# Kernel optimization log

Measured on AMD Instinct MI355X. Metric: run time of the kernel, lower is better.

Reference implementation:

```python
import jax, jax.numpy as jnp
import numpy as np

TEMPERATURE = 0.02
B, T, D = 32, 256, 128


def _l2norm(x):
    return x / jnp.linalg.norm(x, axis=-1, keepdims=True)


def setup_inputs() -> dict:
    key = jax.random.key(0)
    k1, k2, k3, k4, k5, k6 = jax.random.split(key, 6)
    query_single = _l2norm(jax.random.normal(k1, (B, D), dtype=jnp.float32))
    pos_single = _l2norm(jax.random.normal(k2, (B, D), dtype=jnp.float32))
    query_multi = _l2norm(jax.random.normal(k3, (B, T, D), dtype=jnp.float32))
    pos_multi = _l2norm(jax.random.normal(k4, (B, T, D), dtype=jnp.float32))
    # variable-length masks (at least 1 valid token each, like real tokenized batches)
    q_len = jax.random.randint(k5, (B,), T // 4, T + 1)
    p_len = jax.random.randint(k6, (B,), T // 4, T + 1)
    pos = jnp.arange(T)[None, :]
    q_mask = pos < q_len[:, None]
    p_mask = pos < p_len[:, None]
    return {
        "query_single": query_single,
        "pos_single": pos_single,
        "query_multi": query_multi,
        "pos_multi": pos_multi,
        "q_mask": q_mask,
        "p_mask": p_mask,
    }


def _late_interaction_similarity(q_tokens, q_mask, p_tokens, p_mask):
    # All-pairs token similarity: [Bq, Bp, Tq, Tp]
    sim = jnp.einsum("bqd,cpd->bcqp", q_tokens, p_tokens)
    neg = jnp.finfo(sim.dtype).min
    sim = jnp.where(p_mask[None, :, None, :], sim, neg)
    mx = jnp.max(sim, axis=-1)                       # [Bq, Bp, Tq]
    mx = jnp.where(q_mask[:, None, :], mx, 0.0)      # drop invalid query tokens
    s = jnp.sum(mx, axis=-1)                         # [Bq, Bp]
    t_i = jnp.maximum(jnp.sum(q_mask, axis=-1), 1).astype(sim.dtype)  # [Bq]
    return s / t_i[:, None]


def _diag_cross_entropy(logits):
    # labels = arange(B): standard in-batch InfoNCE
    logp = jax.nn.log_softmax(logits, axis=-1)
    return -jnp.mean(jnp.diagonal(logp))


def reference(query_single, pos_single, query_multi, pos_multi, q_mask, p_mask):
    tau = TEMPERATURE
    dense_sim = query_single @ pos_single.T                       # [B, B]
    single_loss = _diag_cross_entropy(dense_sim / tau)

    S_late = _late_interaction_similarity(query_multi, q_mask, pos_multi, p_mask)
    multi_loss = _diag_cross_entropy(S_late / tau)

    dense_probs = jax.nn.softmax(dense_sim / tau, axis=1)
    late_probs = jax.nn.softmax(S_late / tau, axis=1)
    eps = 1e-8
    kl = jnp.mean(jnp.sum(dense_probs * jnp.log((dense_probs + eps) / (late_probs + eps)), axis=1))

    total_loss = single_loss + multi_loss + kl
    return (total_loss, single_loss, multi_loss, kl)
```

## Files before the change

### kernel.cpp

```cpp
#include <hip/hip_runtime.h>
#include <hip/hip_bf16.h>

#define B_SZ 32
#define T_SZ 256
#define D_SZ 128
#define TAU_INV 50.0f

typedef __bf16 bf16x8 __attribute__((ext_vector_type(8)));
typedef float f32x4 __attribute__((ext_vector_type(4)));

__device__ __forceinline__ unsigned short f2bf(float f) {
    union { float f; unsigned int u; } v; v.f = f;
    unsigned int r = v.u + 0x7fffu + ((v.u >> 16) & 1u);
    return (unsigned short)(r >> 16);
}

__device__ __forceinline__ bool mask_is_byte(const void* m) {
    return ((const int*)m)[0] != 1;
}
__device__ __forceinline__ int mget(const void* m, int idx, bool isb) {
    return isb ? (((const unsigned char*)m)[idx] != 0) : (((const int*)m)[idx] != 0);
}

__global__ __launch_bounds__(256) void cvt_prep(
    const float* __restrict__ qsrc, const float* __restrict__ psrc,
    const void* __restrict__ qmask, const void* __restrict__ pmask,
    unsigned short* __restrict__ Qb, unsigned short* __restrict__ Pb,
    float* __restrict__ maddF, float* __restrict__ qmulF,
    int* __restrict__ p_hiA, float* __restrict__ tcntA) {
    const int tid = threadIdx.x;
    const int half = blockIdx.x >> 10;
    if (half < 2) {
        const float* s = half ? psrc : qsrc;
        unsigned short* d = half ? Pb : Qb;
        int i = ((blockIdx.x & 1023) * 256 + tid) * 4;
        float4 v = *(const float4*)(s + i);
        ushort4 o;
        o.x = f2bf(v.x); o.y = f2bf(v.y); o.z = f2bf(v.z); o.w = f2bf(v.w);
        *(ushort4*)(d + i) = o;
        return;
    }
    __shared__ int sl[4], sc[4];
    const bool isb = mask_is_byte(qmask);
    const int r = blockIdx.x - 2048;
    const int t = tid;
    const int pm = mget(pmask, r * T_SZ + t, isb);
    const int qm = mget(qmask, r * T_SZ + t, isb);
    maddF[r * T_SZ + t] = pm ? 0.0f : -1e30f;
    qmulF[r * T_SZ + t] = qm ? 1.0f : 0.0f;
    int lp = pm ? t + 1 : 0, cq = qm;
    #pragma unroll
    for (int off = 1; off < 64; off <<= 1) {
        int o = __shfl_xor(lp, off);
        lp = o > lp ? o : lp;
        cq += __shfl_xor(cq, off);
    }
    if ((tid & 63) == 0) { sl[tid >> 6] = lp; sc[tid >> 6] = cq; }
    __syncthreads();
    if (tid == 0) {
        int LP = sl[0], CQ = sc[0];
        #pragma unroll
        for (int i = 1; i < 4; ++i) { LP = sl[i] > LP ? sl[i] : LP; CQ += sc[i]; }
        p_hiA[r] = LP > 1 ? LP : 1;
        tcntA[r] = (float)(CQ > 1 ? CQ : 1);
    }
}

__global__ __launch_bounds__(512, 4) void late_sim(
    const unsigned short* __restrict__ Qbf, const unsigned short* __restrict__ Pbf,
    const float* __restrict__ maddF, const float* __restrict__ qmulF,
    const int* __restrict__ p_hiA, float* __restrict__ sraw)
{
    __shared__ __align__(16) unsigned char Plds[T_SZ * D_SZ * 2];
    __shared__ float madd[T_SZ];
    __shared__ float qmul[2][T_SZ];
    __shared__ float wsum[2][8];

    const int tid = threadIdx.x;
    const int l   = tid & 63;
    const int w   = tid >> 6;
    const int bid = blockIdx.x;
    const int xcd = bid & 7;
    const int idx = bid >> 3;
    const int bg  = xcd * 2 + (idx >> 5);
    const int c   = idx & 31;
    const int b0  = bg, b1 = bg + 16;
    const int lr  = l & 15;
    const int lg  = l >> 4;

    const int p_hi    = p_hiA[c];
    const int ptmax   = (p_hi + 15) >> 4;
    const int stiters = (p_hi + 31) >> 5;

    const int qrow = w * 32 + (l & 31);
    const bool do0 = __any(qmulF[b0 * T_SZ + qrow] > 0.0f);
    const bool do1 = __any(qmulF[b1 * T_SZ + qrow] > 0.0f);

    bf16x8 qf0[2][4] = {}, qf1[2][4] = {};
    if (do0)
        #pragma unroll
        for (int qt = 0; qt < 2; ++qt)
            #pragma unroll
            for (int k = 0; k < 4; ++k)
                qf0[qt][k] = *(const bf16x8*)(Qbf + b0 * (T_SZ * D_SZ)
                              + (w * 32 + qt * 16 + lr) * D_SZ + k * 32 + lg * 8);
    if (do1)
        #pragma unroll
        for (int qt = 0; qt < 2; ++qt)
            #pragma unroll
            for (int k = 0; k < 4; ++k)
                qf1[qt][k] = *(const bf16x8*)(Qbf + b1 * (T_SZ * D_SZ)
                              + (w * 32 + qt * 16 + lr) * D_SZ + k * 32 + lg * 8);

    {
        const unsigned short* Pc = Pbf + c * (T_SZ * D_SZ);
        for (int it = 0; it < stiters; ++it) {
            int j   = it * 512 + w * 64 + l;
            int row = j >> 4;
            int cj  = j & 15;
            const unsigned short* src = Pc + row * D_SZ + ((cj ^ (row & 7)) << 3);
            __builtin_amdgcn_global_load_lds(
                (const __attribute__((address_space(1))) unsigned int*)src,
                (__attribute__((address_space(3))) unsigned int*)(Plds + (it * 512 + w * 64) * 16),
                16, 0, 0);
        }
    }
    if (tid < 64) {
        *(float4*)(madd + tid * 4) = *(const float4*)(maddF + c * T_SZ + tid * 4);
    } else if (tid < 128) {
        int t = tid - 64;
        *(float4*)(qmul[0] + t * 4) = *(const float4*)(qmulF + b0 * T_SZ + t * 4);
    } else if (tid < 192) {
        int t = tid - 128;
        *(float4*)(qmul[1] + t * 4) = *(const float4*)(qmulF + b1 * T_SZ + t * 4);
    }
    __syncthreads();

    float r00 = -3e38f, r01 = -3e38f, r10 = -3e38f, r11 = -3e38f;

    for (int pt = 0; pt < ptmax; ++pt) {
        f32x4 a00 = {0,0,0,0}, a01 = {0,0,0,0}, a10 = {0,0,0,0}, a11 = {0,0,0,0};
        #pragma unroll
        for (int k = 0; k < 4; ++k) {
            int row = pt * 16 + lr;
            bf16x8 af = *(const bf16x8*)(Plds + row * 256 + (((k * 4 + lg) ^ (row & 7)) << 4));
            if (do0) {
                a00 = __builtin_amdgcn_mfma_f32_16x16x32_bf16(af, qf0[0][k], a00, 0, 0, 0);
                a01 = __builtin_amdgcn_mfma_f32_16x16x32_bf16(af, qf0[1][k], a01, 0, 0, 0);
            }
            if (do1) {
                a10 = __builtin_amdgcn_mfma_f32_16x16x32_bf16(af, qf1[0][k], a10, 0, 0, 0);
                a11 = __builtin_amdgcn_mfma_f32_16x16x32_bf16(af, qf1[1][k], a11, 0, 0, 0);
            }
        }
        float pm0 = madd[pt * 16 + lg * 4 + 0];
        float pm1 = madd[pt * 16 + lg * 4 + 1];
        float pm2 = madd[pt * 16 + lg * 4 + 2];
        float pm3v = madd[pt * 16 + lg * 4 + 3];
        if (do0) {
            r00 = fmaxf(r00, fmaxf(fmaxf(a00[0]+pm0, a00[1]+pm1), fmaxf(a00[2]+pm2, a00[3]+pm3v)));
            r01 = fmaxf(r01, fmaxf(fmaxf(a01[0]+pm0, a01[1]+pm1), fmaxf(a01[2]+pm2, a01[3]+pm3v)));
        }
        if (do1) {
            r10 = fmaxf(r10, fmaxf(fmaxf(a10[0]+pm0, a10[1]+pm1), fmaxf(a10[2]+pm2, a10[3]+pm3v)));
            r11 = fmaxf(r11, fmaxf(fmaxf(a11[0]+pm0, a11[1]+pm1), fmaxf(a11[2]+pm2, a11[3]+pm3v)));
        }
    }

    r00 = fmaxf(r00, __shfl_xor(r00, 16)); r00 = fmaxf(r00, __shfl_xor(r00, 32));
    r01 = fmaxf(r01, __shfl_xor(r01, 16)); r01 = fmaxf(r01, __shfl_xor(r01, 32));
    r10 = fmaxf(r10, __shfl_xor(r10, 16)); r10 = fmaxf(r10, __shfl_xor(r10, 32));
    r11 = fmaxf(r11, __shfl_xor(r11, 16)); r11 = fmaxf(r11, __shfl_xor(r11, 32));

    float t0 = r00 * qmul[0][w * 32 + lr] + r01 * qmul[0][w * 32 + 16 + lr];
    float t1 = r10 * qmul[1][w * 32 + lr] + r11 * qmul[1][w * 32 + 16 + lr];
    #pragma unroll
    for (int off = 32; off > 0; off >>= 1) {
        t0 += __shfl_down(t0, off);
        t1 += __shfl_down(t1, off);
    }
    if (l == 0) { wsum[0][w] = t0 * 0.25f; wsum[1][w] = t1 * 0.25f; }
    __syncthreads();

    if (tid == 0) {
        float s0 = 0.f, s1 = 0.f;
        #pragma unroll
        for (int ww = 0; ww < 8; ++ww) { s0 += wsum[0][ww]; s1 += wsum[1][ww]; }
        sraw[b0 * 32 + c] = s0;
        sraw[b1 * 32 + c] = s1;
    }
}

__global__ __launch_bounds__(256) void loss_row(
    const float* __restrict__ qs, const float* __restrict__ ps,
    const float* __restrict__ sraw, const float* __restrict__ tcntA,
    float* __restrict__ out)
{
    __shared__ float denseL[B_SZ], lateL[B_SZ];
    const int r   = blockIdx.x;
    const int tid = threadIdx.x;
    const int cc  = tid >> 3;
    const int j   = tid & 7;

    {
        const float4* qa = (const float4*)(qs + r  * D_SZ + j * 16);
        const float4* pb = (const float4*)(ps + cc * D_SZ + j * 16);
        float s = 0.f;
        #pragma unroll
        for (int v = 0; v < 4; ++v) {
            float4 q = qa[v], p = pb[v];
            s += q.x * p.x + q.y * p.y + q.z * p.z + q.w * p.w;
        }
        s += __shfl_xor(s, 1);
        s += __shfl_xor(s, 2);
        s += __shfl_xor(s, 4);
        if (j == 0) denseL[cc] = s;
    }
    if (tid < B_SZ) lateL[tid] = sraw[r * 32 + tid] / tcntA[r];
    __syncthreads();

    if (tid >= 32) return;
    const int lane = tid;
    float xd = denseL[lane] * TAU_INV;
    float xl = lateL[lane]  * TAU_INV;
    float md = xd, ml = xl;
    #pragma unroll
    for (int off = 16; off > 0; off >>= 1) {
        md = fmaxf(md, __shfl_xor(md, off));
        ml = fmaxf(ml, __shfl_xor(ml, off));
    }
    float sd = expf(xd - md), sl = expf(xl - ml);
    #pragma unroll
    for (int off = 16; off > 0; off >>= 1) {
        sd += __shfl_xor(sd, off);
        sl += __shfl_xor(sl, off);
    }
    float lsd = md + logf(sd);
    float lsl = ml + logf(sl);
    float pd = expf(xd - lsd);
    float pl = expf(xl - lsl);
    float klt = pd * logf((pd + 1e-8f) / (pl + 1e-8f));
    #pragma unroll
    for (int off = 16; off > 0; off >>= 1) klt += __shfl_xor(klt, off);

    float logpd = xd - lsd;
    float logpl = xl - lsl;
    float dlogd = __shfl(logpd, r);
    float dlogl = __shfl(logpl, r);

    if (lane == 0) {
        const float inv = 1.0f / (float)B_SZ;
        float a = -dlogd * inv;
        float b = -dlogl * inv;
        float k = klt * inv;
        atomicAdd(out + 1, a);
        atomicAdd(out + 2, b);
        atomicAdd(out + 3, k);
        atomicAdd(out + 0, a + b + k);
    }
}

extern "C" void kernel_launch(void* const* d_in, const int* in_sizes, int n_in,
                              void* d_out, int out_size, void* d_ws, size_t ws_size,
                              hipStream_t stream) {
    const float* qs    = (const float*)d_in[0];
    const float* ps    = (const float*)d_in[1];
    const float* qm3   = (const float*)d_in[2];
    const float* pm3   = (const float*)d_in[3];
    const void*  qmask = d_in[4];
    const void*  pmask = d_in[5];
    float* out = (float*)d_out;

    const int NTOK = B_SZ * T_SZ * D_SZ;
    unsigned short* Qbf = (unsigned short*)d_ws;
    unsigned short* Pbf = Qbf + NTOK;
    float* sraw  = (float*)(Pbf + NTOK);
    float* maddF = sraw + 1024;
    float* qmulF = maddF + B_SZ * T_SZ;
    int*   p_hiA = (int*)(qmulF + B_SZ * T_SZ);
    float* tcntA = (float*)(p_hiA + 32);

    hipMemsetAsync(out, 0, 4 * sizeof(float), stream);
    cvt_prep<<<2080, 256, 0, stream>>>(qm3, pm3, qmask, pmask, Qbf, Pbf,
                                       maddF, qmulF, p_hiA, tcntA);
    late_sim<<<512, 512, 0, stream>>>(Qbf, Pbf, maddF, qmulF, p_hiA, sraw);
    loss_row<<<B_SZ, 256, 0, stream>>>(qs, ps, sraw, tcntA, out);
}
```

Measured before the change: 35.73 us.

## Double-buffer two passage blocks per workgroup and coarsen bf16 conversion

The late-interaction kernel now uses 1024-thread workgroups that handle two passage batches each. Each wave covers one query batch, and the second passage tile is loaded into a separate LDS buffer while the first is being computed. The conversion kernel handles eight elements of both Q and P per thread, which cuts the block count. Two 64KB LDS buffers limit occupancy to one block per CU, and the grid shrinks to 256 blocks, which may reduce latency hiding.

Result: faster. 34.28 us, median of 2 (-4.1%).

```diff
diff --git a/kernel.cpp b/kernel.cpp
--- a/kernel.cpp
+++ b/kernel.cpp
@@ -22,27 +22,31 @@
     return isb ? (((const unsigned char*)m)[idx] != 0) : (((const int*)m)[idx] != 0);
 }
 
-__global__ __launch_bounds__(256) void cvt_prep(
+__global__ __launch_bounds__(256) void cvt_prep2(
     const float* __restrict__ qsrc, const float* __restrict__ psrc,
     const void* __restrict__ qmask, const void* __restrict__ pmask,
     unsigned short* __restrict__ Qb, unsigned short* __restrict__ Pb,
     float* __restrict__ maddF, float* __restrict__ qmulF,
     int* __restrict__ p_hiA, float* __restrict__ tcntA) {
     const int tid = threadIdx.x;
-    const int half = blockIdx.x >> 10;
-    if (half < 2) {
-        const float* s = half ? psrc : qsrc;
-        unsigned short* d = half ? Pb : Qb;
-        int i = ((blockIdx.x & 1023) * 256 + tid) * 4;
-        float4 v = *(const float4*)(s + i);
-        ushort4 o;
-        o.x = f2bf(v.x); o.y = f2bf(v.y); o.z = f2bf(v.z); o.w = f2bf(v.w);
-        *(ushort4*)(d + i) = o;
+    if (blockIdx.x < 512) {
+        int i = (blockIdx.x * 256 + tid) * 8;
+        const float4* q4 = (const float4*)(qsrc + i);
+        const float4* p4 = (const float4*)(psrc + i);
+        float4 a0 = q4[0], a1 = q4[1], b0 = p4[0], b1 = p4[1];
+        ushort4 oq0 = { f2bf(a0.x), f2bf(a0.y), f2bf(a0.z), f2bf(a0.w) };
+        ushort4 oq1 = { f2bf(a1.x), f2bf(a1.y), f2bf(a1.z), f2bf(a1.w) };
+        ushort4 op0 = { f2bf(b0.x), f2bf(b0.y), f2bf(b0.z), f2bf(b0.w) };
+        ushort4 op1 = { f2bf(b1.x), f2bf(b1.y), f2bf(b1.z), f2bf(b1.w) };
+        *(ushort4*)(Qb + i)     = oq0;
+        *(ushort4*)(Qb + i + 4) = oq1;
+        *(ushort4*)(Pb + i)     = op0;
+        *(ushort4*)(Pb + i + 4) = op1;
         return;
     }
     __shared__ int sl[4], sc[4];
     const bool isb = mask_is_byte(qmask);
-    const int r = blockIdx.x - 2048;
+    const int r = blockIdx.x - 512;
     const int t = tid;
     const int pm = mget(pmask, r * T_SZ + t, isb);
     const int qm = mget(qmask, r * T_SZ + t, isb);
@@ -66,104 +70,131 @@
     }
 }
 
-__global__ __launch_bounds__(512, 4) void late_sim(
+__global__ __launch_bounds__(1024, 4) void late_sim2(
     const unsigned short* __restrict__ Qbf, const unsigned short* __restrict__ Pbf,
     const float* __restrict__ maddF, const float* __restrict__ qmulF,
     const int* __restrict__ p_hiA, float* __restrict__ sraw)
 {
-    __shared__ __align__(16) unsigned char Plds[T_SZ * D_SZ * 2];
-    __shared__ float madd[T_SZ];
-    __shared__ float qmul[2][T_SZ];
-    __shared__ float wsum[2][8];
+    __shared__ __align__(16) unsigned char Pl[2][T_SZ * D_SZ * 2];
+    __shared__ float maddL[2][T_SZ];
+    __shared__ float qmulL[2][T_SZ];
+    __shared__ float wsum[16][2];
 
     const int tid = threadIdx.x;
     const int l   = tid & 63;
     const int w   = tid >> 6;
     const int bid = blockIdx.x;
     const int xcd = bid & 7;
-    const int idx = bid >> 3;
-    const int bg  = xcd * 2 + (idx >> 5);
-    const int c   = idx & 31;
+    const int j   = bid >> 3;
+    const int bg  = xcd * 2 + (j >> 4);
+    const int cp  = j & 15;
+    const int c0  = cp * 2, c1 = cp * 2 + 1;
     const int b0  = bg, b1 = bg + 16;
     const int lr  = l & 15;
     const int lg  = l >> 4;
-
-    const int p_hi    = p_hiA[c];
-    const int ptmax   = (p_hi + 15) >> 4;
-    const int stiters = (p_hi + 31) >> 5;
-
-    const int qrow = w * 32 + (l & 31);
-    const bool do0 = __any(qmulF[b0 * T_SZ + qrow] > 0.0f);
-    const bool do1 = __any(qmulF[b1 * T_SZ + qrow] > 0.0f);
-
-    bf16x8 qf0[2][4] = {}, qf1[2][4] = {};
-    if (do0)
+    const int wb  = w >> 3;
+    const int myb = wb ? b1 : b0;
+    const int s   = (w & 7) * 32;
+
+    const int p_hi0 = p_hiA[c0], p_hi1 = p_hiA[c1];
+    const int pt0 = (p_hi0 + 15) >> 4, st0 = (p_hi0 + 63) >> 6;
+    const int pt1 = (p_hi1 + 15) >> 4, st1 = (p_hi1 + 63) >> 6;
+
+    const bool dob = __any(qmulF[myb * T_SZ + s + (l & 31)] > 0.0f);
+
+    bf16x8 qf[2][4] = {};
+    if (dob)
         #pragma unroll
         for (int qt = 0; qt < 2; ++qt)
             #pragma unroll
             for (int k = 0; k < 4; ++k)
-                qf0[qt][k] = *(const bf16x8*)(Qbf + b0 * (T_SZ * D_SZ)
-                              + (w * 32 + qt * 16 + lr) * D_SZ + k * 32 + lg * 8);
-    if (do1)
-        #pragma unroll
-        for (int qt = 0; qt < 2; ++qt)
-            #pragma unroll
-            for (int k = 0; k < 4; ++k)
-                qf1[qt][k] = *(const bf16x8*)(Qbf + b1 * (T_SZ * D_SZ)
-                              + (w * 32 + qt * 16 + lr) * D_SZ + k * 32 + lg * 8);
+                qf[qt][k] = *(const bf16x8*)(Qbf + myb * (T_SZ * D_SZ)
+                              + (s + qt * 16 + lr) * D_SZ + k * 32 + lg * 8);
 
     {
-        const unsigned short* Pc = Pbf + c * (T_SZ * D_SZ);
-        for (int it = 0; it < stiters; ++it) {
-            int j   = it * 512 + w * 64 + l;
-            int row = j >> 4;
-            int cj  = j & 15;
+        const unsigned short* Pc = Pbf + c0 * (T_SZ * D_SZ);
+        for (int it = 0; it < st0; ++it) {
+            int m   = it * 1024 + tid;
+            int row = m >> 4;
+            int cj  = m & 15;
             const unsigned short* src = Pc + row * D_SZ + ((cj ^ (row & 7)) << 3);
             __builtin_amdgcn_global_load_lds(
                 (const __attribute__((address_space(1))) unsigned int*)src,
-                (__attribute__((address_space(3))) unsigned int*)(Plds + (it * 512 + w * 64) * 16),
+                (__attribute__((address_space(3))) unsigned int*)(Pl[0] + (it * 1024 + w * 64) * 16),
                 16, 0, 0);
         }
     }
     if (tid < 64) {
-        *(float4*)(madd + tid * 4) = *(const float4*)(maddF + c * T_SZ + tid * 4);
+        *(float4*)(maddL[0] + tid * 4) = *(const float4*)(maddF + c0 * T_SZ + tid * 4);
     } else if (tid < 128) {
         int t = tid - 64;
-        *(float4*)(qmul[0] + t * 4) = *(const float4*)(qmulF + b0 * T_SZ + t * 4);
+        *(float4*)(maddL[1] + t * 4) = *(const float4*)(maddF + c1 * T_SZ + t * 4);
     } else if (tid < 192) {
         int t = tid - 128;
-        *(float4*)(qmul[1] + t * 4) = *(const float4*)(qmulF + b1 * T_SZ + t * 4);
-    }
-    __syncthreads();
-
-    float r00 = -3e38f, r01 = -3e38f, r10 = -3e38f, r11 = -3e38f;
-
-    for (int pt = 0; pt < ptmax; ++pt) {
-        f32x4 a00 = {0,0,0,0}, a01 = {0,0,0,0}, a10 = {0,0,0,0}, a11 = {0,0,0,0};
+        *(float4*)(qmulL[0] + t * 4) = *(const float4*)(qmulF + b0 * T_SZ + t * 4);
+    } else if (tid < 256) {
+        int t = tid - 192;
+        *(float4*)(qmulL[1] + t * 4) = *(const float4*)(qmulF + b1 * T_SZ + t * 4);
+    }
+    __syncthreads();
+
+    {
+        const unsigned short* Pc = Pbf + c1 * (T_SZ * D_SZ);
+        for (int it = 0; it < st1; ++it) {
+            int m   = it * 1024 + tid;
+            int row = m >> 4;
+            int cj  = m & 15;
+            const unsigned short* src = Pc + row * D_SZ + ((cj ^ (row & 7)) << 3);
+            __builtin_amdgcn_global_load_lds(
+                (const __attribute__((address_space(1))) unsigned int*)src,
+                (__attribute__((address_space(3))) unsigned int*)(Pl[1] + (it * 1024 + w * 64) * 16),
+                16, 0, 0);
+        }
+    }
+
+    float r00 = -3e38f, r01 = -3e38f;
+    float r10 = -3e38f, r11 = -3e38f;
+
+    for (int pt = 0; pt < pt0; ++pt) {
+        f32x4 a0 = {0,0,0,0}, a1 = {0,0,0,0};
         #pragma unroll
         for (int k = 0; k < 4; ++k) {
             int row = pt * 16 + lr;
-            bf16x8 af = *(const bf16x8*)(Plds + row * 256 + (((k * 4 + lg) ^ (row & 7)) << 4));
-            if (do0) {
-                a00 = __builtin_amdgcn_mfma_f32_16x16x32_bf16(af, qf0[0][k], a00, 0, 0, 0);
-                a01 = __builtin_amdgcn_mfma_f32_16x16x32_bf16(af, qf0[1][k], a01, 0, 0, 0);
+            bf16x8 af = *(const bf16x8*)(Pl[0] + row * 256 + (((k * 4 + lg) ^ (row & 7)) << 4));
+            if (dob) {
+                a0 = __builtin_amdgcn_mfma_f32_16x16x32_bf16(af, qf[0][k], a0, 0, 0, 0);
+                a1 = __builtin_amdgcn_mfma_f32_16x16x32_bf16(af, qf[1][k], a1, 0, 0, 0);
             }
-            if (do1) {
-                a10 = __builtin_amdgcn_mfma_f32_16x16x32_bf16(af, qf1[0][k], a10, 0, 0, 0);
-                a11 = __builtin_amdgcn_mfma_f32_16x16x32_bf16(af, qf1[1][k], a11, 0, 0, 0);
+        }
+        float pm0 = maddL[0][pt * 16 + lg * 4 + 0];
+        float pm1 = maddL[0][pt * 16 + lg * 4 + 1];
+        float pm2 = maddL[0][pt * 16 + lg * 4 + 2];
+        float pm3 = maddL[0][pt * 16 + lg * 4 + 3];
+        if (dob) {
+            r00 = fmaxf(r00, fmaxf(fmaxf(a0[0]+pm0, a0[1]+pm1), fmaxf(a0[2]+pm2, a0[3]+pm3)));
+            r01 = fmaxf(r01, fmaxf(fmaxf(a1[0]+pm0, a1[1]+pm1), fmaxf(a1[2]+pm2, a1[3]+pm3)));
+        }
+    }
+    __syncthreads();
+
+    for (int pt = 0; pt < pt1; ++pt) {
+        f32x4 a0 = {0,0,0,0}, a1 = {0,0,0,0};
+        #pragma unroll
+        for (int k = 0; k < 4; ++k) {
+            int row = pt * 16 + lr;
+            bf16x8 af = *(const bf16x8*)(Pl[1] + row * 256 + (((k * 4 + lg) ^ (row & 7)) << 4));
+            if (dob) {
+                a0 = __builtin_amdgcn_mfma_f32_16x16x32_bf16(af, qf[0][k], a0, 0, 0, 0);
+                a1 = __builtin_amdgcn_mfma_f32_16x16x32_bf16(af, qf[1][k], a1, 0, 0, 0);
             }
         }
-        float pm0 = madd[pt * 16 + lg * 4 + 0];
-        float pm1 = madd[pt * 16 + lg * 4 + 1];
-        float pm2 = madd[pt * 16 + lg * 4 + 2];
-        float pm3v = madd[pt * 16 + lg * 4 + 3];
-        if (do0) {
-            r00 = fmaxf(r00, fmaxf(fmaxf(a00[0]+pm0, a00[1]+pm1), fmaxf(a00[2]+pm2, a00[3]+pm3v)));
-            r01 = fmaxf(r01, fmaxf(fmaxf(a01[0]+pm0, a01[1]+pm1), fmaxf(a01[2]+pm2, a01[3]+pm3v)));
-        }
-        if (do1) {
-            r10 = fmaxf(r10, fmaxf(fmaxf(a10[0]+pm0, a10[1]+pm1), fmaxf(a10[2]+pm2, a10[3]+pm3v)));
-            r11 = fmaxf(r11, fmaxf(fmaxf(a11[0]+pm0, a11[1]+pm1), fmaxf(a11[2]+pm2, a11[3]+pm3v)));
+        float pm0 = maddL[1][pt * 16 + lg * 4 + 0];
+        float pm1 = maddL[1][pt * 16 + lg * 4 + 1];
+        float pm2 = maddL[1][pt * 16 + lg * 4 + 2];
+        float pm3 = maddL[1][pt * 16 + lg * 4 + 3];
+        if (dob) {
+            r10 = fmaxf(r10, fmaxf(fmaxf(a0[0]+pm0, a0[1]+pm1), fmaxf(a0[2]+pm2, a0[3]+pm3)));
+            r11 = fmaxf(r11, fmaxf(fmaxf(a1[0]+pm0, a1[1]+pm1), fmaxf(a1[2]+pm2, a1[3]+pm3)));
         }
     }
 
@@ -172,22 +203,22 @@
     r10 = fmaxf(r10, __shfl_xor(r10, 16)); r10 = fmaxf(r10, __shfl_xor(r10, 32));
     r11 = fmaxf(r11, __shfl_xor(r11, 16)); r11 = fmaxf(r11, __shfl_xor(r11, 32));
 
-    float t0 = r00 * qmul[0][w * 32 + lr] + r01 * qmul[0][w * 32 + 16 + lr];
-    float t1 = r10 * qmul[1][w * 32 + lr] + r11 * qmul[1][w * 32 + 16 + lr];
+    float t0 = r00 * qmulL[wb][s + lr] + r01 * qmulL[wb][s + 16 + lr];
+    float t1 = r10 * qmulL[wb][s + lr] + r11 * qmulL[wb][s + 16 + lr];
     #pragma unroll
     for (int off = 32; off > 0; off >>= 1) {
         t0 += __shfl_down(t0, off);
         t1 += __shfl_down(t1, off);
     }
-    if (l == 0) { wsum[0][w] = t0 * 0.25f; wsum[1][w] = t1 * 0.25f; }
-    __syncthreads();
-
-    if (tid == 0) {
-        float s0 = 0.f, s1 = 0.f;
-        #pragma unroll
-        for (int ww = 0; ww < 8; ++ww) { s0 += wsum[0][ww]; s1 += wsum[1][ww]; }
-        sraw[b0 * 32 + c] = s0;
-        sraw[b1 * 32 + c] = s1;
+    if (l == 0) { wsum[w][0] = t0 * 0.25f; wsum[w][1] = t1 * 0.25f; }
+    __syncthreads();
+
+    if (tid < 4) {
+        const int bsel = tid >> 1, csel = tid & 1;
+        float sum = 0.f;
+        #pragma unroll
+        for (int ww = 0; ww < 8; ++ww) sum += wsum[bsel * 8 + ww][csel];
+        sraw[(bsel ? b1 : b0) * 32 + (csel ? c1 : c0)] = sum;
     }
 }
 
@@ -281,8 +312,8 @@
     float* tcntA = (float*)(p_hiA + 32);
 
     hipMemsetAsync(out, 0, 4 * sizeof(float), stream);
-    cvt_prep<<<2080, 256, 0, stream>>>(qm3, pm3, qmask, pmask, Qbf, Pbf,
+    cvt_prep2<<<544, 256, 0, stream>>>(qm3, pm3, qmask, pmask, Qbf, Pbf,
                                        maddF, qmulF, p_hiA, tcntA);
-    late_sim<<<512, 512, 0, stream>>>(Qbf, Pbf, maddF, qmulF, p_hiA, sraw);
+    late_sim2<<<256, 1024, 0, stream>>>(Qbf, Pbf, maddF, qmulF, p_hiA, sraw);
     loss_row<<<B_SZ, 256, 0, stream>>>(qs, ps, sraw, tcntA, out);
 }
```

## Fold mask preprocessing into consumers and give each wave one query batch

Applied to the files above, without the earlier changes.

Drops the mask-preprocessing blocks from the conversion kernel, which now processes 8 floats per thread over 512 blocks. The similarity kernel reads raw masks directly to build its shared-memory mask arrays and p_hi, and the loss kernel counts query tokens itself. Each wave now owns one query batch with four 16-row tiles instead of two batches with two tiles each, so skipping a fully masked batch is decided per wave. This removes intermediate mask buffers and a prep phase, at the cost of redundant mask reads across many blocks.

After: 36.12 us. No clear change (+1.1%).

```diff
diff --git a/kernel.cpp b/kernel.cpp
--- a/kernel.cpp
+++ b/kernel.cpp
@@ -22,59 +22,33 @@
     return isb ? (((const unsigned char*)m)[idx] != 0) : (((const int*)m)[idx] != 0);
 }
 
-__global__ __launch_bounds__(256) void cvt_prep(
+__global__ __launch_bounds__(256) void cvt2(
     const float* __restrict__ qsrc, const float* __restrict__ psrc,
+    unsigned short* __restrict__ Qb, unsigned short* __restrict__ Pb) {
+    const int tid = threadIdx.x;
+    int i = (blockIdx.x * 256 + tid) * 8;
+    const float4* q4 = (const float4*)(qsrc + i);
+    const float4* p4 = (const float4*)(psrc + i);
+    float4 a0 = q4[0], a1 = q4[1], b0 = p4[0], b1 = p4[1];
+    ushort4 oq0 = { f2bf(a0.x), f2bf(a0.y), f2bf(a0.z), f2bf(a0.w) };
+    ushort4 oq1 = { f2bf(a1.x), f2bf(a1.y), f2bf(a1.z), f2bf(a1.w) };
+    ushort4 op0 = { f2bf(b0.x), f2bf(b0.y), f2bf(b0.z), f2bf(b0.w) };
+    ushort4 op1 = { f2bf(b1.x), f2bf(b1.y), f2bf(b1.z), f2bf(b1.w) };
+    *(ushort4*)(Qb + i)     = oq0;
+    *(ushort4*)(Qb + i + 4) = oq1;
+    *(ushort4*)(Pb + i)     = op0;
+    *(ushort4*)(Pb + i + 4) = op1;
+}
+
+__global__ __launch_bounds__(512, 4) void late3(
+    const unsigned short* __restrict__ Qbf, const unsigned short* __restrict__ Pbf,
     const void* __restrict__ qmask, const void* __restrict__ pmask,
-    unsigned short* __restrict__ Qb, unsigned short* __restrict__ Pb,
-    float* __restrict__ maddF, float* __restrict__ qmulF,
-    int* __restrict__ p_hiA, float* __restrict__ tcntA) {
-    const int tid = threadIdx.x;
-    const int half = blockIdx.x >> 10;
-    if (half < 2) {
-        const float* s = half ? psrc : qsrc;
-        unsigned short* d = half ? Pb : Qb;
-        int i = ((blockIdx.x & 1023) * 256 + tid) * 4;
-        float4 v = *(const float4*)(s + i);
-        ushort4 o;
-        o.x = f2bf(v.x); o.y = f2bf(v.y); o.z = f2bf(v.z); o.w = f2bf(v.w);
-        *(ushort4*)(d + i) = o;
-        return;
-    }
-    __shared__ int sl[4], sc[4];
-    const bool isb = mask_is_byte(qmask);
-    const int r = blockIdx.x - 2048;
-    const int t = tid;
-    const int pm = mget(pmask, r * T_SZ + t, isb);
-    const int qm = mget(qmask, r * T_SZ + t, isb);
-    maddF[r * T_SZ + t] = pm ? 0.0f : -1e30f;
-    qmulF[r * T_SZ + t] = qm ? 1.0f : 0.0f;
-    int lp = pm ? t + 1 : 0, cq = qm;
-    #pragma unroll
-    for (int off = 1; off < 64; off <<= 1) {
-        int o = __shfl_xor(lp, off);
-        lp = o > lp ? o : lp;
-        cq += __shfl_xor(cq, off);
-    }
-    if ((tid & 63) == 0) { sl[tid >> 6] = lp; sc[tid >> 6] = cq; }
-    __syncthreads();
-    if (tid == 0) {
-        int LP = sl[0], CQ = sc[0];
-        #pragma unroll
-        for (int i = 1; i < 4; ++i) { LP = sl[i] > LP ? sl[i] : LP; CQ += sc[i]; }
-        p_hiA[r] = LP > 1 ? LP : 1;
-        tcntA[r] = (float)(CQ > 1 ? CQ : 1);
-    }
-}
-
-__global__ __launch_bounds__(512, 4) void late_sim(
-    const unsigned short* __restrict__ Qbf, const unsigned short* __restrict__ Pbf,
-    const float* __restrict__ maddF, const float* __restrict__ qmulF,
-    const int* __restrict__ p_hiA, float* __restrict__ sraw)
+    float* __restrict__ sraw)
 {
     __shared__ __align__(16) unsigned char Plds[T_SZ * D_SZ * 2];
     __shared__ float madd[T_SZ];
     __shared__ float qmul[2][T_SZ];
-    __shared__ float wsum[2][8];
+    __shared__ float wsum[8];
 
     const int tid = threadIdx.x;
     const int l   = tid & 63;
@@ -87,37 +61,47 @@
     const int b0  = bg, b1 = bg + 16;
     const int lr  = l & 15;
     const int lg  = l >> 4;
-
-    const int p_hi    = p_hiA[c];
+    const int wb  = w >> 2;
+    const int myb = wb ? b1 : b0;
+    const int s   = (w & 3) * 64;
+
+    const bool isb = mask_is_byte(qmask);
+
+    int p_hi;
+    {
+        int v = 0;
+        #pragma unroll
+        for (int j2 = 0; j2 < 4; ++j2) {
+            int t = l * 4 + j2;
+            if (mget(pmask, c * T_SZ + t, isb)) v = t + 1;
+        }
+        #pragma unroll
+        for (int off = 1; off < 64; off <<= 1) {
+            int o = __shfl_xor(v, off);
+            v = o > v ? o : v;
+        }
+        p_hi = v > 1 ? v : 1;
+    }
     const int ptmax   = (p_hi + 15) >> 4;
     const int stiters = (p_hi + 31) >> 5;
 
-    const int qrow = w * 32 + (l & 31);
-    const bool do0 = __any(qmulF[b0 * T_SZ + qrow] > 0.0f);
-    const bool do1 = __any(qmulF[b1 * T_SZ + qrow] > 0.0f);
-
-    bf16x8 qf0[2][4] = {}, qf1[2][4] = {};
-    if (do0)
-        #pragma unroll
-        for (int qt = 0; qt < 2; ++qt)
+    const bool dob = __any(mget(qmask, myb * T_SZ + s + l, isb));
+
+    bf16x8 qf[4][4] = {};
+    if (dob)
+        #pragma unroll
+        for (int qt = 0; qt < 4; ++qt)
             #pragma unroll
             for (int k = 0; k < 4; ++k)
-                qf0[qt][k] = *(const bf16x8*)(Qbf + b0 * (T_SZ * D_SZ)
-                              + (w * 32 + qt * 16 + lr) * D_SZ + k * 32 + lg * 8);
-    if (do1)
-        #pragma unroll
-        for (int qt = 0; qt < 2; ++qt)
-            #pragma unroll
-            for (int k = 0; k < 4; ++k)
-                qf1[qt][k] = *(const bf16x8*)(Qbf + b1 * (T_SZ * D_SZ)
-                              + (w * 32 + qt * 16 + lr) * D_SZ + k * 32 + lg * 8);
+                qf[qt][k] = *(const bf16x8*)(Qbf + myb * (T_SZ * D_SZ)
+                              + (s + qt * 16 + lr) * D_SZ + k * 32 + lg * 8);
 
     {
         const unsigned short* Pc = Pbf + c * (T_SZ * D_SZ);
         for (int it = 0; it < stiters; ++it) {
-            int j   = it * 512 + w * 64 + l;
-            int row = j >> 4;
-            int cj  = j & 15;
+            int m   = it * 512 + w * 64 + l;
+            int row = m >> 4;
+            int cj  = m & 15;
             const unsigned short* src = Pc + row * D_SZ + ((cj ^ (row & 7)) << 3);
             __builtin_amdgcn_global_load_lds(
                 (const __attribute__((address_space(1))) unsigned int*)src,
@@ -125,82 +109,73 @@
                 16, 0, 0);
         }
     }
-    if (tid < 64) {
-        *(float4*)(madd + tid * 4) = *(const float4*)(maddF + c * T_SZ + tid * 4);
-    } else if (tid < 128) {
-        int t = tid - 64;
-        *(float4*)(qmul[0] + t * 4) = *(const float4*)(qmulF + b0 * T_SZ + t * 4);
-    } else if (tid < 192) {
-        int t = tid - 128;
-        *(float4*)(qmul[1] + t * 4) = *(const float4*)(qmulF + b1 * T_SZ + t * 4);
+    if (tid < 256) {
+        madd[tid]    = mget(pmask, c  * T_SZ + tid, isb) ? 0.0f : -1e30f;
+        qmul[0][tid] = mget(qmask, b0 * T_SZ + tid, isb) ? 1.0f : 0.0f;
+    } else {
+        int t = tid - 256;
+        qmul[1][t]   = mget(qmask, b1 * T_SZ + t, isb) ? 1.0f : 0.0f;
     }
     __syncthreads();
 
-    float r00 = -3e38f, r01 = -3e38f, r10 = -3e38f, r11 = -3e38f;
+    float r0 = -3e38f, r1 = -3e38f, r2 = -3e38f, r3 = -3e38f;
 
     for (int pt = 0; pt < ptmax; ++pt) {
-        f32x4 a00 = {0,0,0,0}, a01 = {0,0,0,0}, a10 = {0,0,0,0}, a11 = {0,0,0,0};
+        f32x4 a0 = {0,0,0,0}, a1 = {0,0,0,0}, a2 = {0,0,0,0}, a3 = {0,0,0,0};
         #pragma unroll
         for (int k = 0; k < 4; ++k) {
             int row = pt * 16 + lr;
             bf16x8 af = *(const bf16x8*)(Plds + row * 256 + (((k * 4 + lg) ^ (row & 7)) << 4));
-            if (do0) {
-                a00 = __builtin_amdgcn_mfma_f32_16x16x32_bf16(af, qf0[0][k], a00, 0, 0, 0);
-                a01 = __builtin_amdgcn_mfma_f32_16x16x32_bf16(af, qf0[1][k], a01, 0, 0, 0);
-            }
-            if (do1) {
-                a10 = __builtin_amdgcn_mfma_f32_16x16x32_bf16(af, qf1[0][k], a10, 0, 0, 0);
-                a11 = __builtin_amdgcn_mfma_f32_16x16x32_bf16(af, qf1[1][k], a11, 0, 0, 0);
+            if (dob) {
+                a0 = __builtin_amdgcn_mfma_f32_16x16x32_bf16(af, qf[0][k], a0, 0, 0, 0);
+                a1 = __builtin_amdgcn_mfma_f32_16x16x32_bf16(af, qf[1][k], a1, 0, 0, 0);
+                a2 = __builtin_amdgcn_mfma_f32_16x16x32_bf16(af, qf[2][k], a2, 0, 0, 0);
+                a3 = __builtin_amdgcn_mfma_f32_16x16x32_bf16(af, qf[3][k], a3, 0, 0, 0);
             }
         }
         float pm0 = madd[pt * 16 + lg * 4 + 0];
         float pm1 = madd[pt * 16 + lg * 4 + 1];
         float pm2 = madd[pt * 16 + lg * 4 + 2];
-        float pm3v = madd[pt * 16 + lg * 4 + 3];
-        if (do0) {
-            r00 = fmaxf(r00, fmaxf(fmaxf(a00[0]+pm0, a00[1]+pm1), fmaxf(a00[2]+pm2, a00[3]+pm3v)));
-            r01 = fmaxf(r01, fmaxf(fmaxf(a01[0]+pm0, a01[1]+pm1), fmaxf(a01[2]+pm2, a01[3]+pm3v)));
-        }
-        if (do1) {
-            r10 = fmaxf(r10, fmaxf(fmaxf(a10[0]+pm0, a10[1]+pm1), fmaxf(a10[2]+pm2, a10[3]+pm3v)));
-            r11 = fmaxf(r11, fmaxf(fmaxf(a11[0]+pm0, a11[1]+pm1), fmaxf(a11[2]+pm2, a11[3]+pm3v)));
-        }
-    }
-
-    r00 = fmaxf(r00, __shfl_xor(r00, 16)); r00 = fmaxf(r00, __shfl_xor(r00, 32));
-    r01 = fmaxf(r01, __shfl_xor(r01, 16)); r01 = fmaxf(r01, __shfl_xor(r01, 32));
-    r10 = fmaxf(r10, __shfl_xor(r10, 16)); r10 = fmaxf(r10, __shfl_xor(r10, 32));
-    r11 = fmaxf(r11, __shfl_xor(r11, 16)); r11 = fmaxf(r11, __shfl_xor(r11, 32));
-
-    float t0 = r00 * qmul[0][w * 32 + lr] + r01 * qmul[0][w * 32 + 16 + lr];
-    float t1 = r10 * qmul[1][w * 32 + lr] + r11 * qmul[1][w * 32 + 16 + lr];
-    #pragma unroll
-    for (int off = 32; off > 0; off >>= 1) {
-        t0 += __shfl_down(t0, off);
-        t1 += __shfl_down(t1, off);
-    }
-    if (l == 0) { wsum[0][w] = t0 * 0.25f; wsum[1][w] = t1 * 0.25f; }
+        float pm3 = madd[pt * 16 + lg * 4 + 3];
+        if (dob) {
+            r0 = fmaxf(r0, fmaxf(fmaxf(a0[0]+pm0, a0[1]+pm1), fmaxf(a0[2]+pm2, a0[3]+pm3)));
+            r1 = fmaxf(r1, fmaxf(fmaxf(a1[0]+pm0, a1[1]+pm1), fmaxf(a1[2]+pm2, a1[3]+pm3)));
+            r2 = fmaxf(r2, fmaxf(fmaxf(a2[0]+pm0, a2[1]+pm1), fmaxf(a2[2]+pm2, a2[3]+pm3)));
+            r3 = fmaxf(r3, fmaxf(fmaxf(a3[0]+pm0, a3[1]+pm1), fmaxf(a3[2]+pm2, a3[3]+pm3)));
+        }
+    }
+
+    r0 = fmaxf(r0, __shfl_xor(r0, 16)); r0 = fmaxf(r0, __shfl_xor(r0, 32));
+    r1 = fmaxf(r1, __shfl_xor(r1, 16)); r1 = fmaxf(r1, __shfl_xor(r1, 32));
+    r2 = fmaxf(r2, __shfl_xor(r2, 16)); r2 = fmaxf(r2, __shfl_xor(r2, 32));
+    r3 = fmaxf(r3, __shfl_xor(r3, 16)); r3 = fmaxf(r3, __shfl_xor(r3, 32));
+
+    float t0 = r0 * qmul[wb][s + lr]      + r1 * qmul[wb][s + 16 + lr]
+             + r2 * qmul[wb][s + 32 + lr] + r3 * qmul[wb][s + 48 + lr];
+    #pragma unroll
+    for (int off = 32; off > 0; off >>= 1) t0 += __shfl_down(t0, off);
+    if (l == 0) wsum[w] = t0 * 0.25f;
     __syncthreads();
 
-    if (tid == 0) {
-        float s0 = 0.f, s1 = 0.f;
-        #pragma unroll
-        for (int ww = 0; ww < 8; ++ww) { s0 += wsum[0][ww]; s1 += wsum[1][ww]; }
-        sraw[b0 * 32 + c] = s0;
-        sraw[b1 * 32 + c] = s1;
-    }
-}
-
-__global__ __launch_bounds__(256) void loss_row(
+    if (tid < 2) {
+        float sum = wsum[tid * 4] + wsum[tid * 4 + 1]
+                  + wsum[tid * 4 + 2] + wsum[tid * 4 + 3];
+        sraw[(tid ? b1 : b0) * 32 + c] = sum;
+    }
+}
+
+__global__ __launch_bounds__(256) void loss_row2(
     const float* __restrict__ qs, const float* __restrict__ ps,
-    const float* __restrict__ sraw, const float* __restrict__ tcntA,
+    const float* __restrict__ sraw, const void* __restrict__ qmask,
     float* __restrict__ out)
 {
-    __shared__ float denseL[B_SZ], lateL[B_SZ];
+    __shared__ float denseL[B_SZ];
+    __shared__ float stcnt;
     const int r   = blockIdx.x;
     const int tid = threadIdx.x;
     const int cc  = tid >> 3;
     const int j   = tid & 7;
+    const bool isb = mask_is_byte(qmask);
 
     {
         const float4* qa = (const float4*)(qs + r  * D_SZ + j * 16);
@@ -216,13 +191,21 @@
         s += __shfl_xor(s, 4);
         if (j == 0) denseL[cc] = s;
     }
-    if (tid < B_SZ) lateL[tid] = sraw[r * 32 + tid] / tcntA[r];
+    if (tid < 32) {
+        int cnt = 0;
+        #pragma unroll
+        for (int k = 0; k < 8; ++k)
+            cnt += mget(qmask, r * T_SZ + tid + k * 32, isb);
+        #pragma unroll
+        for (int off = 1; off < 32; off <<= 1) cnt += __shfl_xor(cnt, off);
+        if (tid == 0) stcnt = (float)(cnt > 1 ? cnt : 1);
+    }
     __syncthreads();
 
     if (tid >= 32) return;
     const int lane = tid;
     float xd = denseL[lane] * TAU_INV;
-    float xl = lateL[lane]  * TAU_INV;
+    float xl = (sraw[r * 32 + lane] / stcnt) * TAU_INV;
     float md = xd, ml = xl;
     #pragma unroll
     for (int off = 16; off > 0; off >>= 1) {
@@ -274,15 +257,10 @@
     const int NTOK = B_SZ * T_SZ * D_SZ;
     unsigned short* Qbf = (unsigned short*)d_ws;
     unsigned short* Pbf = Qbf + NTOK;
-    float* sraw  = (float*)(Pbf + NTOK);
-    float* maddF = sraw + 1024;
-    float* qmulF = maddF + B_SZ * T_SZ;
-    int*   p_hiA = (int*)(qmulF + B_SZ * T_SZ);
-    float* tcntA = (float*)(p_hiA + 32);
+    float* sraw = (float*)(Pbf + NTOK);
 
     hipMemsetAsync(out, 0, 4 * sizeof(float), stream);
-    cvt_prep<<<2080, 256, 0, stream>>>(qm3, pm3, qmask, pmask, Qbf, Pbf,
-                                       maddF, qmulF, p_hiA, tcntA);
-    late_sim<<<512, 512, 0, stream>>>(Qbf, Pbf, maddF, qmulF, p_hiA, sraw);
-    loss_row<<<B_SZ, 256, 0, stream>>>(qs, ps, sraw, tcntA, out);
-}
+    cvt2<<<512, 256, 0, stream>>>(qm3, pm3, Qbf, Pbf);
+    late3<<<512, 512, 0, stream>>>(Qbf, Pbf, qmask, pmask, sraw);
+    loss_row2<<<B_SZ, 256, 0, stream>>>(qs, ps, sraw, qmask, out);
+}
```
